# Kernel tuning notes

Hardware: AMD Instinct MI355X
Metric: run time of the kernel (lower is better)

## Reference

```python
import jax, jax.numpy as jnp
import numpy as np

STRIDES = (8, 16, 32)
FEAT_SIZES = ((80, 80), (40, 40), (20, 20))  # (h, w) per level for 640x640 input
OFFSET = 0.5
NMS_K = 300
IOU_THR = 0.65
EPS = 1e-7


def make_priors():
    """MlvlPointGenerator.grid_priors with with_stride=True, flattened over levels."""
    pts, strs = [], []
    for (h, w), s in zip(FEAT_SIZES, STRIDES):
        xs = (jnp.arange(w, dtype=jnp.float32) + OFFSET) * s
        ys = (jnp.arange(h, dtype=jnp.float32) + OFFSET) * s
        yy, xx = jnp.meshgrid(ys, xs, indexing='ij')
        pts.append(jnp.stack([xx.reshape(-1), yy.reshape(-1)], -1))
        strs.append(jnp.full((h * w, 2), float(s), dtype=jnp.float32))
    return jnp.concatenate(pts, 0), jnp.concatenate(strs, 0)  # [N,2], [N,2]


def pairwise_iou(boxes):  # boxes [K,4] xyxy
    area = jnp.clip(boxes[:, 2] - boxes[:, 0], 0) * jnp.clip(boxes[:, 3] - boxes[:, 1], 0)
    lt = jnp.maximum(boxes[:, None, :2], boxes[None, :, :2])
    rb = jnp.minimum(boxes[:, None, 2:], boxes[None, :, 2:])
    wh = jnp.clip(rb - lt, 0)
    inter = wh[..., 0] * wh[..., 1]
    union = area[:, None] + area[None, :] - inter
    return inter / (union + EPS)


def nms_keep(boxes):  # boxes [K,4] sorted by descending score -> bool keep mask [K]
    K = boxes.shape[0]
    iou = pairwise_iou(boxes)
    idx = jnp.arange(K)

    def body(i, keep):
        sup = (iou[i] > IOU_THR) & (idx > i) & keep[i]
        return keep & ~sup

    return jax.lax.fori_loop(0, K, body, jnp.ones((K,), dtype=bool))


def setup_inputs() -> dict:
    key = jax.random.key(0)
    k1, k2, k3, k4, k5 = jax.random.split(key, 5)
    B, N, K = 128, 8400, 17
    return {
        'cls_scores': jax.random.normal(k1, (B, N, 1), jnp.float32),
        'bbox_preds': jax.random.normal(k2, (B, N, 4), jnp.float32),
        'objectness': jax.random.normal(k3, (B, N), jnp.float32),
        'kpt_offsets': jax.random.normal(k4, (B, N, K, 2), jnp.float32),
        'kpt_vis_preds': jax.random.normal(k5, (B, N, K), jnp.float32),
    }


def reference(cls_scores, bbox_preds, objectness, kpt_offsets, kpt_vis_preds):
    priors, strides = make_priors()  # [N,2] each
    # bbox decode: center-offset + exp wh, YOLOX style
    xy = bbox_preds[..., :2] * strides + priors            # [B,N,2]
    wh = jnp.exp(bbox_preds[..., 2:4]) * strides           # [B,N,2]
    boxes = jnp.concatenate([xy - wh * 0.5, xy + wh * 0.5], -1)  # [B,N,4]
    scores = jax.nn.sigmoid(cls_scores[..., 0]) * jax.nn.sigmoid(objectness)  # [B,N]
    # keypoint decode
    kpts = kpt_offsets * strides[:, None, :] + priors[:, None, :]  # [B,N,K,2]
    B, N, K, _ = kpts.shape
    kpts_flat = kpts.reshape(B, N, K * 2)
    vis = jax.nn.sigmoid(kpt_vis_preds)                    # [B,N,K]
    # fixed-size top-k pre-NMS selection
    top_vals, top_idx = jax.lax.top_k(scores, NMS_K)       # [B,NMS_K]
    gather = lambda x: jnp.take_along_axis(x, top_idx[..., None], axis=1)
    boxes_k = gather(boxes)       # [B,NMS_K,4]
    kpts_k = gather(kpts_flat)    # [B,NMS_K,2K]
    vis_k = gather(vis)           # [B,NMS_K,K]
    keep = jax.vmap(nms_keep)(boxes_k)                      # [B,NMS_K] bool
    final_scores = top_vals * keep.astype(top_vals.dtype)
    # [B, NMS_K, 4 + 1 + 2K + K]
    return jnp.concatenate([boxes_k, final_scores[..., None], kpts_k, vis_k], -1)
```

## Files before the change

### kernel.cpp

```cpp
#include <hip/hip_runtime.h>
#include <math.h>

#define BATCH 128
#define NANCH 8400
#define NMSK  300
#define KPT   17
#define OUTC  56
#define CAND  1024
#define NTHR  1024
#define NBIN  8192
#define BSHIFT 19

__device__ __forceinline__ void prior_of(int i, float& stride, float& cx, float& cy) {
    int row, col;
    if (i < 6400)      { stride = 8.0f;  row = i / 80;              col = i - row * 80; }
    else if (i < 8000) { int ii = i - 6400; stride = 16.0f; row = ii / 40; col = ii - row * 40; }
    else               { int ii = i - 8000; stride = 32.0f; row = ii / 20; col = ii - row * 20; }
    cx = ((float)col + 0.5f) * stride;
    cy = ((float)row + 0.5f) * stride;
}

__global__ __launch_bounds__(256) void scores_kernel(
    const float* __restrict__ cls, const float* __restrict__ obj,
    unsigned int* __restrict__ sc)
{
    int i = blockIdx.x * 256 + threadIdx.x;
    float4 cv = ((const float4*)cls)[i];
    float4 ov = ((const float4*)obj)[i];
    float sa0 = 1.0f / (1.0f + (float)exp(-(double)cv.x));
    float sa1 = 1.0f / (1.0f + (float)exp(-(double)cv.y));
    float sa2 = 1.0f / (1.0f + (float)exp(-(double)cv.z));
    float sa3 = 1.0f / (1.0f + (float)exp(-(double)cv.w));
    float so0 = 1.0f / (1.0f + (float)exp(-(double)ov.x));
    float so1 = 1.0f / (1.0f + (float)exp(-(double)ov.y));
    float so2 = 1.0f / (1.0f + (float)exp(-(double)ov.z));
    float so3 = 1.0f / (1.0f + (float)exp(-(double)ov.w));
    uint4 r;
    r.x = __float_as_uint(sa0 * so0);
    r.y = __float_as_uint(sa1 * so1);
    r.z = __float_as_uint(sa2 * so2);
    r.w = __float_as_uint(sa3 * so3);
    ((uint4*)sc)[i] = r;
}

__global__ __launch_bounds__(NTHR) void select_kernel(
    const unsigned int* __restrict__ sc_g, const float* __restrict__ bbox,
    float* __restrict__ out, int* __restrict__ sidx_g)
{
    const int b = blockIdx.x;
    const int tid = threadIdx.x;
    const int lane = tid & 63;
    const int wv = tid >> 6;

    __shared__ __align__(16) unsigned int sc[NANCH];
    __shared__ __align__(16) unsigned int hist[NBIN];
    __shared__ unsigned int wtot[16], wab[16];
    __shared__ unsigned int sh_pivot, sh_cnt;
    __shared__ unsigned long long ckey[CAND];
    __shared__ float bx1[NMSK], by1[NMSK], bx2[NMSK], by2[NMSK], area[NMSK];
    __shared__ float sval[NMSK];
    __shared__ int   sidx[NMSK];
    __shared__ unsigned long long supl[NMSK * 6];
    __shared__ unsigned long long keepw[5];

    {
        const uint4* s4 = (const uint4*)(sc_g + (size_t)b * NANCH);
        uint4* d4 = (uint4*)sc;
        for (int i = tid; i < NANCH / 4; i += NTHR) d4[i] = s4[i];
        uint4 z; z.x = z.y = z.z = z.w = 0u;
        uint4* h4 = (uint4*)hist;
        for (int i = tid; i < NBIN / 4; i += NTHR) h4[i] = z;
        if (tid == 0) sh_cnt = 0u;
    }
    __syncthreads();

    for (int i = tid; i < NANCH; i += NTHR) atomicAdd(&hist[sc[i] >> BSHIFT], 1u);
    __syncthreads();

    unsigned int s7[8];
    {
        uint4 a = ((uint4*)hist)[2 * tid];
        uint4 c = ((uint4*)hist)[2 * tid + 1];
        unsigned int h0 = a.x, h1 = a.y, h2 = a.z, h3 = a.w;
        unsigned int h4 = c.x, h5 = c.y, h6 = c.z, h7 = c.w;
        s7[7] = h7;
        s7[6] = s7[7] + h6; s7[5] = s7[6] + h5; s7[4] = s7[5] + h4;
        s7[3] = s7[4] + h3; s7[2] = s7[3] + h2; s7[1] = s7[2] + h1;
        s7[0] = s7[1] + h0;
    }
    unsigned int T = s7[0];
    unsigned int v = T;
    #pragma unroll
    for (int d = 1; d < 64; d <<= 1) {
        unsigned int t2 = (unsigned int)__shfl_down((int)v, d, 64);
        if (lane + d < 64) v += t2;
    }
    unsigned int aiw = v - T;
    if (lane == 0) wtot[wv] = v;
    __syncthreads();
    if (tid < 16) {
        unsigned int wa = 0;
        for (int q = tid + 1; q < 16; ++q) wa += wtot[q];
        wab[tid] = wa;
    }
    __syncthreads();
    {
        unsigned int ag = wab[wv] + aiw;
        #pragma unroll
        for (int k = 0; k < 8; ++k) hist[8 * tid + k] = ag + s7[k];
    }
    __syncthreads();

    #pragma unroll
    for (int k = 0; k < 8; ++k) {
        unsigned int bin = 8 * (unsigned)tid + k;
        unsigned int ge = hist[bin];
        unsigned int gn = (bin < NBIN - 1) ? hist[bin + 1] : 0u;
        if (ge >= NMSK && gn < NMSK) sh_pivot = bin;
    }
    __syncthreads();
    unsigned int pivot_bits = sh_pivot << BSHIFT;

    for (int base = 0; base < NANCH; base += NTHR) {
        int i = base + tid;
        bool valid = (i < NANCH);
        unsigned int key = valid ? sc[i] : 0u;
        bool pred = valid && (key >= pivot_bits);
        unsigned long long m = __ballot(pred);
        unsigned int cnt = (unsigned int)__popcll(m);
        unsigned int wbase = 0u;
        if (lane == 0 && cnt) wbase = atomicAdd(&sh_cnt, cnt);
        wbase = (unsigned int)__shfl((int)wbase, 0, 64);
        if (pred) {
            unsigned int p = wbase + (unsigned int)__popcll(m & ((1ull << lane) - 1ull));
            if (p < CAND)
                ckey[p] = ((unsigned long long)key << 32)
                        | (unsigned long long)(0xFFFFFFFFu - (unsigned int)i);
        }
    }
    __syncthreads();
    unsigned int M = sh_cnt; if (M > CAND) M = CAND;

    if (tid < (int)M) {
        unsigned long long mine = ckey[tid];
        int rank = 0;
        for (unsigned int t2 = 0; t2 < M; ++t2) rank += (ckey[t2] > mine) ? 1 : 0;
        if (rank < NMSK) {
            sidx[rank] = (int)(0xFFFFFFFFu - (unsigned int)(mine & 0xFFFFFFFFull));
            sval[rank] = __uint_as_float((unsigned int)(mine >> 32));
        }
    }
    __syncthreads();

    if (tid < NMSK) {
        int j = tid;
        int i = sidx[j];
        float stride, cx, cy;
        prior_of(i, stride, cx, cy);
        float4 bb = *(const float4*)(bbox + ((size_t)b * NANCH + (size_t)i) * 4);
        float x = bb.x * stride + cx;
        float y = bb.y * stride + cy;
        float w = expf(bb.z) * stride;
        float h = expf(bb.w) * stride;
        float x1 = x - 0.5f * w, y1 = y - 0.5f * h;
        float x2 = x + 0.5f * w, y2 = y + 0.5f * h;
        bx1[j] = x1; by1[j] = y1; bx2[j] = x2; by2[j] = y2;
        area[j] = fmaxf(x2 - x1, 0.0f) * fmaxf(y2 - y1, 0.0f);
    }
    __syncthreads();

    for (int t = tid; t < NMSK * 5; t += NTHR) {
        int w = t / NMSK;
        int i = t - w * NMSK;
        int jlo = w * 64; if (jlo < i + 1) jlo = i + 1;
        int jhi = w * 64 + 64; if (jhi > NMSK) jhi = NMSK;
        unsigned long long m = 0;
        float ax1 = bx1[i], ay1 = by1[i], ax2 = bx2[i], ay2 = by2[i], aa = area[i];
        for (int j = jlo; j < jhi; ++j) {
            float lx = fmaxf(ax1, bx1[j]);
            float ly = fmaxf(ay1, by1[j]);
            float rx = fminf(ax2, bx2[j]);
            float ry = fminf(ay2, by2[j]);
            float iw = fmaxf(rx - lx, 0.0f);
            float ih = fmaxf(ry - ly, 0.0f);
            float inter = iw * ih;
            float iou = inter / (aa + area[j] - inter + 1e-7f);
            if (iou > 0.65f) m |= 1ull << (j & 63);
        }
        supl[i * 6 + w] = m;
    }
    __syncthreads();

    if (tid < 64) {
        int j = tid;
        unsigned long long keep0 = ~0ull, keep1 = ~0ull, keep2 = ~0ull, keep3 = ~0ull;
        unsigned long long keep4 = (1ull << (NMSK - 256)) - 1ull;
        #define CHUNK(C, KC, IMAX) { \
            int r = (C) * 64 + j; \
            unsigned int lo0=0,hi0=0,lo1=0,hi1=0,lo2=0,hi2=0,lo3=0,hi3=0,lo4=0,hi4=0; \
            if (r < NMSK) { \
                unsigned long long w0 = supl[r*6+0], w1 = supl[r*6+1], w2 = supl[r*6+2]; \
                unsigned long long w3 = supl[r*6+3], w4 = supl[r*6+4]; \
                lo0=(unsigned int)w0; hi0=(unsigned int)(w0>>32); \
                lo1=(unsigned int)w1; hi1=(unsigned int)(w1>>32); \
                lo2=(unsigned int)w2; hi2=(unsigned int)(w2>>32); \
                lo3=(unsigned int)w3; hi3=(unsigned int)(w3>>32); \
                lo4=(unsigned int)w4; hi4=(unsigned int)(w4>>32); } \
            for (int bi = 0; bi < (IMAX); ++bi) { \
                if ((KC >> bi) & 1ull) { \
                    unsigned long long s0 = ((unsigned long long)__builtin_amdgcn_readlane(hi0,bi)<<32) | __builtin_amdgcn_readlane(lo0,bi); \
                    unsigned long long s1 = ((unsigned long long)__builtin_amdgcn_readlane(hi1,bi)<<32) | __builtin_amdgcn_readlane(lo1,bi); \
                    unsigned long long s2 = ((unsigned long long)__builtin_amdgcn_readlane(hi2,bi)<<32) | __builtin_amdgcn_readlane(lo2,bi); \
                    unsigned long long s3 = ((unsigned long long)__builtin_amdgcn_readlane(hi3,bi)<<32) | __builtin_amdgcn_readlane(lo3,bi); \
                    unsigned long long s4 = ((unsigned long long)__builtin_amdgcn_readlane(hi4,bi)<<32) | __builtin_amdgcn_readlane(lo4,bi); \
                    keep0 &= ~s0; keep1 &= ~s1; keep2 &= ~s2; keep3 &= ~s3; keep4 &= ~s4; } } }
        CHUNK(0, keep0, 64)
        CHUNK(1, keep1, 64)
        CHUNK(2, keep2, 64)
        CHUNK(3, keep3, 64)
        CHUNK(4, keep4, NMSK - 256)
        #undef CHUNK
        if (j == 0) { keepw[0]=keep0; keepw[1]=keep1; keepw[2]=keep2; keepw[3]=keep3; keepw[4]=keep4; }
    } else {
        int* sg = sidx_g + (size_t)b * NMSK;
        float* ob = out + (size_t)b * NMSK * OUTC;
        for (int t = tid - 64; t < NMSK; t += NTHR - 64) sg[t] = sidx[t];
        for (int t = tid - 64; t < NMSK * 4; t += NTHR - 64) {
            int j = t >> 2, ci = t & 3;
            float vv = (ci == 0) ? bx1[j] : (ci == 1) ? by1[j] : (ci == 2) ? bx2[j] : by2[j];
            ob[j * OUTC + ci] = vv;
        }
    }
    __syncthreads();

    if (tid < NMSK) {
        bool kp = (keepw[tid >> 6] >> (tid & 63)) & 1ull;
        out[(size_t)b * NMSK * OUTC + (size_t)tid * OUTC + 4] = kp ? sval[tid] : 0.0f;
    }
}

__global__ __launch_bounds__(512) void kpt_kernel(
    const int* __restrict__ sidx_g, const float* __restrict__ kofs,
    const float* __restrict__ kvis, float* __restrict__ out)
{
    const int b = blockIdx.x >> 1;
    const int h = blockIdx.x & 1;
    const int tid = threadIdx.x;
    __shared__ int si[NMSK];
    if (tid < NMSK) si[tid] = sidx_g[(size_t)b * NMSK + tid];
    __syncthreads();
    const float* kof = kofs + (size_t)b * NANCH * 34;
    const float* kvi = kvis + (size_t)b * NANCH * KPT;
    float* ob = out + (size_t)b * NMSK * OUTC;
    const int half = (NMSK * 51) / 2;
    const int e0 = h * half;
    for (int e = e0 + tid; e < e0 + half; e += 512) {
        int j  = e / 51;
        int ci = e - j * 51;
        int i  = si[j];
        float stride, cx, cy;
        prior_of(i, stride, cx, cy);
        float v;
        if (ci < 34) {
            float off = kof[(size_t)i * 34 + ci];
            v = off * stride + ((ci & 1) ? cy : cx);
        } else {
            float x = kvi[(size_t)i * KPT + (ci - 34)];
            v = 1.0f / (1.0f + expf(-x));
        }
        ob[j * OUTC + 5 + ci] = v;
    }
}

extern "C" void kernel_launch(void* const* d_in, const int* in_sizes, int n_in,
                              void* d_out, int out_size, void* d_ws, size_t ws_size,
                              hipStream_t stream) {
    const float* cls  = (const float*)d_in[0];
    const float* bbox = (const float*)d_in[1];
    const float* obj  = (const float*)d_in[2];
    const float* kofs = (const float*)d_in[3];
    const float* kvis = (const float*)d_in[4];
    float* out = (float*)d_out;

    unsigned int* sc = (unsigned int*)d_ws;
    int* sidx_g = (int*)((char*)d_ws + (size_t)BATCH * NANCH * sizeof(unsigned int));

    scores_kernel<<<(BATCH * NANCH / 4) / 256, 256, 0, stream>>>(cls, obj, sc);
    select_kernel<<<BATCH, NTHR, 0, stream>>>(sc, bbox, out, sidx_g);
    kpt_kernel<<<BATCH * 2, 512, 0, stream>>>(sidx_g, kofs, kvis, out);
}
```

Before: 325.7 us.

## Fuse score, select, NMS and keypoint kernels into one role-split kernel

```diff
diff --git a/kernel.cpp b/kernel.cpp
--- a/kernel.cpp
+++ b/kernel.cpp
@@ -20,37 +20,16 @@
     cy = ((float)row + 0.5f) * stride;
 }
 
-__global__ __launch_bounds__(256) void scores_kernel(
+__global__ __launch_bounds__(NTHR) void fused_kernel(
     const float* __restrict__ cls, const float* __restrict__ obj,
-    unsigned int* __restrict__ sc)
+    const float* __restrict__ bbox, const float* __restrict__ kofs,
+    const float* __restrict__ kvis, float* __restrict__ out)
 {
-    int i = blockIdx.x * 256 + threadIdx.x;
-    float4 cv = ((const float4*)cls)[i];
-    float4 ov = ((const float4*)obj)[i];
-    float sa0 = 1.0f / (1.0f + (float)exp(-(double)cv.x));
-    float sa1 = 1.0f / (1.0f + (float)exp(-(double)cv.y));
-    float sa2 = 1.0f / (1.0f + (float)exp(-(double)cv.z));
-    float sa3 = 1.0f / (1.0f + (float)exp(-(double)cv.w));
-    float so0 = 1.0f / (1.0f + (float)exp(-(double)ov.x));
-    float so1 = 1.0f / (1.0f + (float)exp(-(double)ov.y));
-    float so2 = 1.0f / (1.0f + (float)exp(-(double)ov.z));
-    float so3 = 1.0f / (1.0f + (float)exp(-(double)ov.w));
-    uint4 r;
-    r.x = __float_as_uint(sa0 * so0);
-    r.y = __float_as_uint(sa1 * so1);
-    r.z = __float_as_uint(sa2 * so2);
-    r.w = __float_as_uint(sa3 * so3);
-    ((uint4*)sc)[i] = r;
-}
-
-__global__ __launch_bounds__(NTHR) void select_kernel(
-    const unsigned int* __restrict__ sc_g, const float* __restrict__ bbox,
-    float* __restrict__ out, int* __restrict__ sidx_g)
-{
-    const int b = blockIdx.x;
-    const int tid = threadIdx.x;
+    const int b    = blockIdx.x >> 1;
+    const int role = blockIdx.x & 1;
+    const int tid  = threadIdx.x;
     const int lane = tid & 63;
-    const int wv = tid >> 6;
+    const int wv   = tid >> 6;
 
     __shared__ __align__(16) unsigned int sc[NANCH];
     __shared__ __align__(16) unsigned int hist[NBIN];
@@ -58,15 +37,30 @@
     __shared__ unsigned int sh_pivot, sh_cnt;
     __shared__ unsigned long long ckey[CAND];
     __shared__ float bx1[NMSK], by1[NMSK], bx2[NMSK], by2[NMSK], area[NMSK];
-    __shared__ float sval[NMSK];
+    __shared__ float sval[NMSK], pst[NMSK], ppx[NMSK], ppy[NMSK];
     __shared__ int   sidx[NMSK];
     __shared__ unsigned long long supl[NMSK * 6];
     __shared__ unsigned long long keepw[5];
 
     {
-        const uint4* s4 = (const uint4*)(sc_g + (size_t)b * NANCH);
-        uint4* d4 = (uint4*)sc;
-        for (int i = tid; i < NANCH / 4; i += NTHR) d4[i] = s4[i];
+        const float4* c4 = (const float4*)(cls + (size_t)b * NANCH);
+        const float4* o4 = (const float4*)(obj + (size_t)b * NANCH);
+        for (int i = tid; i < NANCH / 4; i += NTHR) {
+            float4 cv = c4[i];
+            float4 ov = o4[i];
+            float sa0 = 1.0f / (1.0f + (float)exp(-(double)cv.x));
+            float sa1 = 1.0f / (1.0f + (float)exp(-(double)cv.y));
+            float sa2 = 1.0f / (1.0f + (float)exp(-(double)cv.z));
+            float sa3 = 1.0f / (1.0f + (float)exp(-(double)cv.w));
+            float so0 = 1.0f / (1.0f + (float)exp(-(double)ov.x));
+            float so1 = 1.0f / (1.0f + (float)exp(-(double)ov.y));
+            float so2 = 1.0f / (1.0f + (float)exp(-(double)ov.z));
+            float so3 = 1.0f / (1.0f + (float)exp(-(double)ov.w));
+            sc[4 * i + 0] = __float_as_uint(sa0 * so0);
+            sc[4 * i + 1] = __float_as_uint(sa1 * so1);
+            sc[4 * i + 2] = __float_as_uint(sa2 * so2);
+            sc[4 * i + 3] = __float_as_uint(sa3 * so3);
+        }
         uint4 z; z.x = z.y = z.z = z.w = 0u;
         uint4* h4 = (uint4*)hist;
         for (int i = tid; i < NBIN / 4; i += NTHR) h4[i] = z;
@@ -152,123 +146,116 @@
     }
     __syncthreads();
 
-    if (tid < NMSK) {
-        int j = tid;
-        int i = sidx[j];
-        float stride, cx, cy;
-        prior_of(i, stride, cx, cy);
-        float4 bb = *(const float4*)(bbox + ((size_t)b * NANCH + (size_t)i) * 4);
-        float x = bb.x * stride + cx;
-        float y = bb.y * stride + cy;
-        float w = expf(bb.z) * stride;
-        float h = expf(bb.w) * stride;
-        float x1 = x - 0.5f * w, y1 = y - 0.5f * h;
-        float x2 = x + 0.5f * w, y2 = y + 0.5f * h;
-        bx1[j] = x1; by1[j] = y1; bx2[j] = x2; by2[j] = y2;
-        area[j] = fmaxf(x2 - x1, 0.0f) * fmaxf(y2 - y1, 0.0f);
-    }
-    __syncthreads();
-
-    for (int t = tid; t < NMSK * 5; t += NTHR) {
-        int w = t / NMSK;
-        int i = t - w * NMSK;
-        int jlo = w * 64; if (jlo < i + 1) jlo = i + 1;
-        int jhi = w * 64 + 64; if (jhi > NMSK) jhi = NMSK;
-        unsigned long long m = 0;
-        float ax1 = bx1[i], ay1 = by1[i], ax2 = bx2[i], ay2 = by2[i], aa = area[i];
-        for (int j = jlo; j < jhi; ++j) {
-            float lx = fmaxf(ax1, bx1[j]);
-            float ly = fmaxf(ay1, by1[j]);
-            float rx = fminf(ax2, bx2[j]);
-            float ry = fminf(ay2, by2[j]);
-            float iw = fmaxf(rx - lx, 0.0f);
-            float ih = fmaxf(ry - ly, 0.0f);
-            float inter = iw * ih;
-            float iou = inter / (aa + area[j] - inter + 1e-7f);
-            if (iou > 0.65f) m |= 1ull << (j & 63);
-        }
-        supl[i * 6 + w] = m;
-    }
-    __syncthreads();
-
-    if (tid < 64) {
-        int j = tid;
-        unsigned long long keep0 = ~0ull, keep1 = ~0ull, keep2 = ~0ull, keep3 = ~0ull;
-        unsigned long long keep4 = (1ull << (NMSK - 256)) - 1ull;
-        #define CHUNK(C, KC, IMAX) { \
-            int r = (C) * 64 + j; \
-            unsigned int lo0=0,hi0=0,lo1=0,hi1=0,lo2=0,hi2=0,lo3=0,hi3=0,lo4=0,hi4=0; \
-            if (r < NMSK) { \
-                unsigned long long w0 = supl[r*6+0], w1 = supl[r*6+1], w2 = supl[r*6+2]; \
-                unsigned long long w3 = supl[r*6+3], w4 = supl[r*6+4]; \
-                lo0=(unsigned int)w0; hi0=(unsigned int)(w0>>32); \
-                lo1=(unsigned int)w1; hi1=(unsigned int)(w1>>32); \
-                lo2=(unsigned int)w2; hi2=(unsigned int)(w2>>32); \
-                lo3=(unsigned int)w3; hi3=(unsigned int)(w3>>32); \
-                lo4=(unsigned int)w4; hi4=(unsigned int)(w4>>32); } \
-            for (int bi = 0; bi < (IMAX); ++bi) { \
-                if ((KC >> bi) & 1ull) { \
-                    unsigned long long s0 = ((unsigned long long)__builtin_amdgcn_readlane(hi0,bi)<<32) | __builtin_amdgcn_readlane(lo0,bi); \
-                    unsigned long long s1 = ((unsigned long long)__builtin_amdgcn_readlane(hi1,bi)<<32) | __builtin_amdgcn_readlane(lo1,bi); \
-                    unsigned long long s2 = ((unsigned long long)__builtin_amdgcn_readlane(hi2,bi)<<32) | __builtin_amdgcn_readlane(lo2,bi); \
-                    unsigned long long s3 = ((unsigned long long)__builtin_amdgcn_readlane(hi3,bi)<<32) | __builtin_amdgcn_readlane(lo3,bi); \
-                    unsigned long long s4 = ((unsigned long long)__builtin_amdgcn_readlane(hi4,bi)<<32) | __builtin_amdgcn_readlane(lo4,bi); \
-                    keep0 &= ~s0; keep1 &= ~s1; keep2 &= ~s2; keep3 &= ~s3; keep4 &= ~s4; } } }
-        CHUNK(0, keep0, 64)
-        CHUNK(1, keep1, 64)
-        CHUNK(2, keep2, 64)
-        CHUNK(3, keep3, 64)
-        CHUNK(4, keep4, NMSK - 256)
-        #undef CHUNK
-        if (j == 0) { keepw[0]=keep0; keepw[1]=keep1; keepw[2]=keep2; keepw[3]=keep3; keepw[4]=keep4; }
+    if (role == 0) {
+        if (tid < NMSK) {
+            int j = tid;
+            int i = sidx[j];
+            float stride, cx, cy;
+            prior_of(i, stride, cx, cy);
+            float4 bb = *(const float4*)(bbox + ((size_t)b * NANCH + (size_t)i) * 4);
+            float x = bb.x * stride + cx;
+            float y = bb.y * stride + cy;
+            float w = expf(bb.z) * stride;
+            float h = expf(bb.w) * stride;
+            float x1 = x - 0.5f * w, y1 = y - 0.5f * h;
+            float x2 = x + 0.5f * w, y2 = y + 0.5f * h;
+            bx1[j] = x1; by1[j] = y1; bx2[j] = x2; by2[j] = y2;
+            area[j] = fmaxf(x2 - x1, 0.0f) * fmaxf(y2 - y1, 0.0f);
+        }
+        __syncthreads();
+
+        for (int t = tid; t < NMSK * 5; t += NTHR) {
+            int w = t / NMSK;
+            int i = t - w * NMSK;
+            int jlo = w * 64; if (jlo < i + 1) jlo = i + 1;
+            int jhi = w * 64 + 64; if (jhi > NMSK) jhi = NMSK;
+            unsigned long long m = 0;
+            float ax1 = bx1[i], ay1 = by1[i], ax2 = bx2[i], ay2 = by2[i], aa = area[i];
+            for (int j = jlo; j < jhi; ++j) {
+                float lx = fmaxf(ax1, bx1[j]);
+                float ly = fmaxf(ay1, by1[j]);
+                float rx = fminf(ax2, bx2[j]);
+                float ry = fminf(ay2, by2[j]);
+                float iw = fmaxf(rx - lx, 0.0f);
+                float ih = fmaxf(ry - ly, 0.0f);
+                float inter = iw * ih;
+                float iou = inter / (aa + area[j] - inter + 1e-7f);
+                if (iou > 0.65f) m |= 1ull << (j & 63);
+            }
+            supl[i * 6 + w] = m;
+        }
+        __syncthreads();
+
+        if (tid < 64) {
+            int j = tid;
+            unsigned long long keep0 = ~0ull, keep1 = ~0ull, keep2 = ~0ull, keep3 = ~0ull;
+            unsigned long long keep4 = (1ull << (NMSK - 256)) - 1ull;
+            #define CHUNK(C, KC, IMAX) { \
+                int r = (C) * 64 + j; \
+                unsigned int lo0=0,hi0=0,lo1=0,hi1=0,lo2=0,hi2=0,lo3=0,hi3=0,lo4=0,hi4=0; \
+                if (r < NMSK) { \
+                    unsigned long long w0 = supl[r*6+0], w1 = supl[r*6+1], w2 = supl[r*6+2]; \
+                    unsigned long long w3 = supl[r*6+3], w4 = supl[r*6+4]; \
+                    lo0=(unsigned int)w0; hi0=(unsigned int)(w0>>32); \
+                    lo1=(unsigned int)w1; hi1=(unsigned int)(w1>>32); \
+                    lo2=(unsigned int)w2; hi2=(unsigned int)(w2>>32); \
+                    lo3=(unsigned int)w3; hi3=(unsigned int)(w3>>32); \
+                    lo4=(unsigned int)w4; hi4=(unsigned int)(w4>>32); } \
+                for (int bi = 0; bi < (IMAX); ++bi) { \
+                    if ((KC >> bi) & 1ull) { \
+                        unsigned long long s0 = ((unsigned long long)__builtin_amdgcn_readlane(hi0,bi)<<32) | __builtin_amdgcn_readlane(lo0,bi); \
+                        unsigned long long s1 = ((unsigned long long)__builtin_amdgcn_readlane(hi1,bi)<<32) | __builtin_amdgcn_readlane(lo1,bi); \
+                        unsigned long long s2 = ((unsigned long long)__builtin_amdgcn_readlane(hi2,bi)<<32) | __builtin_amdgcn_readlane(lo2,bi); \
+                        unsigned long long s3 = ((unsigned long long)__builtin_amdgcn_readlane(hi3,bi)<<32) | __builtin_amdgcn_readlane(lo3,bi); \
+                        unsigned long long s4 = ((unsigned long long)__builtin_amdgcn_readlane(hi4,bi)<<32) | __builtin_amdgcn_readlane(lo4,bi); \
+                        keep0 &= ~s0; keep1 &= ~s1; keep2 &= ~s2; keep3 &= ~s3; keep4 &= ~s4; } } }
+            CHUNK(0, keep0, 64)
+            CHUNK(1, keep1, 64)
+            CHUNK(2, keep2, 64)
+            CHUNK(3, keep3, 64)
+            CHUNK(4, keep4, NMSK - 256)
+            #undef CHUNK
+            if (j == 0) { keepw[0]=keep0; keepw[1]=keep1; keepw[2]=keep2; keepw[3]=keep3; keepw[4]=keep4; }
+        } else {
+            float* ob = out + (size_t)b * NMSK * OUTC;
+            for (int t = tid - 64; t < NMSK * 4; t += NTHR - 64) {
+                int j = t >> 2, ci = t & 3;
+                float vv = (ci == 0) ? bx1[j] : (ci == 1) ? by1[j] : (ci == 2) ? bx2[j] : by2[j];
+                ob[j * OUTC + ci] = vv;
+            }
+        }
+        __syncthreads();
+
+        if (tid < NMSK) {
+            bool kp = (keepw[tid >> 6] >> (tid & 63)) & 1ull;
+            out[(size_t)b * NMSK * OUTC + (size_t)tid * OUTC + 4] = kp ? sval[tid] : 0.0f;
+        }
     } else {
-        int* sg = sidx_g + (size_t)b * NMSK;
+        if (tid < NMSK) {
+            int i = sidx[tid];
+            float stride, cx, cy;
+            prior_of(i, stride, cx, cy);
+            pst[tid] = stride; ppx[tid] = cx; ppy[tid] = cy;
+        }
+        __syncthreads();
+
+        const float* kof = kofs + (size_t)b * NANCH * 34;
+        const float* kvi = kvis + (size_t)b * NANCH * KPT;
         float* ob = out + (size_t)b * NMSK * OUTC;
-        for (int t = tid - 64; t < NMSK; t += NTHR - 64) sg[t] = sidx[t];
-        for (int t = tid - 64; t < NMSK * 4; t += NTHR - 64) {
-            int j = t >> 2, ci = t & 3;
-            float vv = (ci == 0) ? bx1[j] : (ci == 1) ? by1[j] : (ci == 2) ? bx2[j] : by2[j];
-            ob[j * OUTC + ci] = vv;
-        }
-    }
-    __syncthreads();
-
-    if (tid < NMSK) {
-        bool kp = (keepw[tid >> 6] >> (tid & 63)) & 1ull;
-        out[(size_t)b * NMSK * OUTC + (size_t)tid * OUTC + 4] = kp ? sval[tid] : 0.0f;
-    }
-}
-
-__global__ __launch_bounds__(512) void kpt_kernel(
-    const int* __restrict__ sidx_g, const float* __restrict__ kofs,
-    const float* __restrict__ kvis, float* __restrict__ out)
-{
-    const int b = blockIdx.x >> 1;
-    const int h = blockIdx.x & 1;
-    const int tid = threadIdx.x;
-    __shared__ int si[NMSK];
-    if (tid < NMSK) si[tid] = sidx_g[(size_t)b * NMSK + tid];
-    __syncthreads();
-    const float* kof = kofs + (size_t)b * NANCH * 34;
-    const float* kvi = kvis + (size_t)b * NANCH * KPT;
-    float* ob = out + (size_t)b * NMSK * OUTC;
-    const int half = (NMSK * 51) / 2;
-    const int e0 = h * half;
-    for (int e = e0 + tid; e < e0 + half; e += 512) {
-        int j  = e / 51;
-        int ci = e - j * 51;
-        int i  = si[j];
-        float stride, cx, cy;
-        prior_of(i, stride, cx, cy);
-        float v;
-        if (ci < 34) {
-            float off = kof[(size_t)i * 34 + ci];
-            v = off * stride + ((ci & 1) ? cy : cx);
-        } else {
-            float x = kvi[(size_t)i * KPT + (ci - 34)];
-            v = 1.0f / (1.0f + expf(-x));
-        }
-        ob[j * OUTC + 5 + ci] = v;
+        for (int e = tid; e < NMSK * 51; e += NTHR) {
+            int j  = e / 51;
+            int ci = e - j * 51;
+            int i  = sidx[j];
+            float vv;
+            if (ci < 34) {
+                float off = kof[(size_t)i * 34 + ci];
+                vv = off * pst[j] + ((ci & 1) ? ppy[j] : ppx[j]);
+            } else {
+                float x = kvi[(size_t)i * KPT + (ci - 34)];
+                vv = 1.0f / (1.0f + expf(-x));
+            }
+            ob[j * OUTC + 5 + ci] = vv;
+        }
     }
 }
 
@@ -282,10 +269,7 @@
     const float* kvis = (const float*)d_in[4];
     float* out = (float*)d_out;
 
-    unsigned int* sc = (unsigned int*)d_ws;
-    int* sidx_g = (int*)((char*)d_ws + (size_t)BATCH * NANCH * sizeof(unsigned int));
-
-    scores_kernel<<<(BATCH * NANCH / 4) / 256, 256, 0, stream>>>(cls, obj, sc);
-    select_kernel<<<BATCH, NTHR, 0, stream>>>(sc, bbox, out, sidx_g);
-    kpt_kernel<<<BATCH * 2, 512, 0, stream>>>(sidx_g, kofs, kvis, out);
+    (void)d_ws; (void)ws_size;
+
+    fused_kernel<<<BATCH * 2, NTHR, 0, stream>>>(cls, obj, bbox, kofs, kvis, out);
 }
```

Result: faster. 296.6 us (-9.0%).
